# Kernel optimization log

Measured on AMD Instinct MI355X. Metric: run time of the kernel, lower is better.

## Reference

```python
import jax, jax.numpy as jnp
import numpy as np

DIM_IN, DIM_OUT, DIM_CTX = 128, 256, 259
B, N, S_CTX = 32, 2048, 1
BN_EPS = 1e-5


def setup_inputs() -> dict:
    key = jax.random.key(0)
    ks = jax.random.split(key, 12)
    s = 0.02
    return {
        "ctx": jax.random.normal(ks[0], (B, S_CTX, DIM_CTX), jnp.float32),
        "x": jax.random.normal(ks[1], (B, N, DIM_IN), jnp.float32),
        "W_layer": jax.random.normal(ks[2], (DIM_OUT, DIM_IN), jnp.float32) * s,
        "b_layer": jax.random.normal(ks[3], (DIM_OUT,), jnp.float32) * s,
        "W_hbias": jax.random.normal(ks[4], (DIM_OUT, DIM_CTX), jnp.float32) * s,
        "W_gate": jax.random.normal(ks[5], (DIM_OUT, DIM_CTX), jnp.float32) * s,
        "b_gate": jax.random.normal(ks[6], (DIM_OUT,), jnp.float32) * s,
        "W_k": jax.random.normal(ks[7], (DIM_OUT, DIM_CTX - 3), jnp.float32) * s,
        "W_v": jax.random.normal(ks[8], (DIM_OUT, DIM_CTX - 3), jnp.float32) * s,
        "W_tc": jax.random.normal(ks[9], (DIM_OUT, DIM_OUT), jnp.float32) * s,
        "b_tc": jax.random.normal(ks[10], (DIM_OUT,), jnp.float32) * s,
        "bn_gamma": jnp.ones((N,), jnp.float32),
        "bn_beta": jnp.zeros((N,), jnp.float32),
    }


def reference(ctx, x, W_layer, b_layer, W_hbias, W_gate, b_gate, W_k, W_v, W_tc, b_tc, bn_gamma, bn_beta):
    # FiLM gate / bias from context: [B, 1, dim_out]
    gate = jax.nn.sigmoid(jnp.einsum('bsc,oc->bso', ctx, W_gate) + b_gate)
    bias = jnp.einsum('bsc,oc->bso', ctx, W_hbias)

    # main linear: [B, N, dim_out]
    x1 = jnp.einsum('bni,oi->bno', x, W_layer) + b_layer

    # channel attention from shape context (drop last 3 ctx dims)
    shape = ctx[:, :, : ctx.shape[2] - 3]                      # [B, S, C-3]
    shape_k = jnp.einsum('bsc,oc->bos', shape, W_k)            # [B, dim_out, S]
    shape_v = jnp.einsum('bsc,oc->bso', shape, W_v)            # [B, S, dim_out]
    energy = jnp.einsum('bos,bse->boe', shape_k, shape_v)      # [B, dim_out, dim_out]
    attention = jax.nn.softmax(energy, axis=-1)
    attention = attention / (1e-9 + attention.sum(axis=1, keepdims=True))

    # channel mixing: [B, N, dim_out]
    x_r = jnp.einsum('bno,boe->bne', x1, attention)

    # trans_conv + BatchNorm1d(N) (train-mode batch stats over dims (0, 2)) + ReLU
    t = jnp.einsum('bno,eo->bne', x1 - x_r, W_tc) + b_tc       # [B, N, dim_out]
    mean = t.mean(axis=(0, 2), keepdims=True)                  # per point-channel
    var = t.var(axis=(0, 2), keepdims=True)                    # biased variance
    t = (t - mean) * jax.lax.rsqrt(var + BN_EPS)
    t = t * bn_gamma[None, :, None] + bn_beta[None, :, None]
    x_r = jax.nn.relu(t)

    xo = x1 + x_r
    return xo * gate + bias
```

## Files before the change

### kernel.cpp

```cpp
#include <hip/hip_runtime.h>
#include <hip/hip_bf16.h>

#define BB   32
#define NN   2048
#define DIN  128
#define DOUT 256
#define DCTX 259

#define OFF_AB   0u
#define OFF_WMB  16777216u
#define OFF_WLB  17301504u
#define OFF_WLTB 17317888u
#define OFF_WTCB 17334272u
#define OFF_G    17367040u
#define OFF_HB   17375232u
#define OFF_TB   17383424u
#define OFF_P1   17655296u
#define OFF_P2   17720832u
#define OFF_KS   17786368u
#define OFF_VS   17794560u

typedef short bf16x8 __attribute__((ext_vector_type(8)));
typedef float f32x4  __attribute__((ext_vector_type(4)));

static __device__ inline unsigned short f2bf(float f) {
    __hip_bfloat16 h = __float2bfloat16(f);
    return *(unsigned short*)&h;
}
static __device__ inline float bf2f(unsigned short u) {
    unsigned v = ((unsigned)u) << 16;
    float f;
    __builtin_memcpy(&f, &v, 4);
    return f;
}

__global__ __launch_bounds__(256) void kW(const float* __restrict__ Wl,
                                          const float* __restrict__ Wtc,
                                          const float* __restrict__ Wk,
                                          const float* __restrict__ Wv,
                                          const float* __restrict__ Wg,
                                          const float* __restrict__ Whb,
                                          const float* __restrict__ ctx,
                                          const float* __restrict__ bg,
                                          float* __restrict__ ws) {
    const unsigned bb = blockIdx.x, t = threadIdx.x;
    __shared__ float ctxs[32][260];
    __shared__ float wt[16][260];

    if (bb < 8u) {
        unsigned base = bb * 8192u;
        unsigned short* dst = (unsigned short*)(ws + OFF_WTCB);
#pragma unroll
        for (int j = 0; j < 32; j++) {
            unsigned i = base + (unsigned)j * 256u + t;
            dst[i] = f2bf(Wtc[i]);
        }
        return;
    } else if (bb == 8u) {
        unsigned short* dst = (unsigned short*)(ws + OFF_WLTB);
        for (unsigned idx = t; idx < 32768u; idx += 256u) {
            unsigned i = idx >> 8, o = idx & 255u;
            dst[idx] = f2bf(Wl[o * 128u + i]);
        }
        return;
    } else if (bb == 9u) {
        unsigned short* dst = (unsigned short*)(ws + OFF_WLB);
        for (unsigned idx = t; idx < 32768u; idx += 256u) dst[idx] = f2bf(Wl[idx]);
        return;
    }

    const int j = bb - 10;
    const int m = j >> 4;
    const int o0 = (j & 15) * 16;
    const float* Wm; int C;
    if (m == 0)      { Wm = Wk;  C = 256; }
    else if (m == 1) { Wm = Wv;  C = 256; }
    else if (m == 2) { Wm = Wg;  C = DCTX; }
    else             { Wm = Whb; C = DCTX; }

    for (int i = t; i < 32 * 260; i += 256) {
        int b2 = i / 260, c = i - b2 * 260;
        ctxs[b2][c] = (c < DCTX) ? ctx[b2 * DCTX + c] : 0.f;
    }
    for (int i = t; i < 16 * C; i += 256) {
        int r = i / C, c = i - r * C;
        wt[r][c] = Wm[(size_t)(o0 + r) * C + c];
    }
    __syncthreads();

    const int ol = t & 15, b2 = t >> 4;
    float s0 = 0.f, s1 = 0.f;
#pragma unroll 8
    for (int c = 0; c < C; c++) {
        float w = wt[ol][c];
        s0 += w * ctxs[b2][c];
        s1 += w * ctxs[b2 + 16][c];
    }
    const int o = o0 + ol;
    if (m == 0) {
        ws[OFF_KS + b2 * DOUT + o] = s0;
        ws[OFF_KS + (b2 + 16) * DOUT + o] = s1;
    } else if (m == 1) {
        ws[OFF_VS + b2 * DOUT + o] = s0;
        ws[OFF_VS + (b2 + 16) * DOUT + o] = s1;
    } else if (m == 2) {
        float bgo = bg[o];
        ws[OFF_G + b2 * DOUT + o] = 1.f / (1.f + __expf(-(s0 + bgo)));
        ws[OFF_G + (b2 + 16) * DOUT + o] = 1.f / (1.f + __expf(-(s1 + bgo)));
    } else {
        ws[OFF_HB + b2 * DOUT + o] = s0;
        ws[OFF_HB + (b2 + 16) * DOUT + o] = s1;
    }
}

__global__ __launch_bounds__(1024) void kP(float* __restrict__ ws) {
    const int b = blockIdx.x, t = threadIdx.x;
    const int o = t & 255, q = t >> 8;
    __shared__ __align__(16) float ks[256], vs[256], rms[256], ris[256];
    __shared__ float pm[1024], ps[1024];
    if (t < 256)            ks[t] = ws[OFF_KS + b * DOUT + t];
    else if (t < 512)       vs[t - 256] = ws[OFF_VS + b * DOUT + (t - 256)];
    __syncthreads();

    const float ko = ks[o];
    const float4* vs4 = (const float4*)vs;
    float pmax = -1e30f;
#pragma unroll 4
    for (int j = q * 16; j < q * 16 + 16; j++) {
        float4 v = vs4[j];
        pmax = fmaxf(pmax, fmaxf(fmaxf(ko * v.x, ko * v.y), fmaxf(ko * v.z, ko * v.w)));
    }
    pm[q * 256 + o] = pmax;
    __syncthreads();
    float m = fmaxf(fmaxf(pm[o], pm[256 + o]), fmaxf(pm[512 + o], pm[768 + o]));
    float psum = 0.f;
#pragma unroll 4
    for (int j = q * 16; j < q * 16 + 16; j++) {
        float4 v = vs4[j];
        psum += __expf(ko * v.x - m) + __expf(ko * v.y - m)
              + __expf(ko * v.z - m) + __expf(ko * v.w - m);
    }
    ps[q * 256 + o] = psum;
    __syncthreads();
    float ri = 1.f / (ps[o] + ps[256 + o] + ps[512 + o] + ps[768 + o]);
    if (q == 0) { rms[o] = m; ris[o] = ri; }
    __syncthreads();

    const float ve = vs[o];
    float cp = 0.f;
#pragma unroll 4
    for (int o2 = q * 64; o2 < q * 64 + 64; o2++)
        cp += __expf(ks[o2] * ve - rms[o2]) * ris[o2];
    pm[q * 256 + o] = cp;
    __syncthreads();
    float ci = 1.f / (1e-9f + pm[o] + pm[256 + o] + pm[512 + o] + pm[768 + o]);
    unsigned short* Ab = (unsigned short*)(ws + OFF_AB) + (size_t)b * 65536u;
#pragma unroll 4
    for (int o2 = q * 64; o2 < q * 64 + 64; o2++) {
        float a = __expf(ks[o2] * ve - rms[o2]) * ris[o2] * ci;
        Ab[o2 * 256 + o] = f2bf(a);
    }
}

__global__ __launch_bounds__(512) void k45(const float* __restrict__ bl,
                                           const float* __restrict__ btc,
                                           float* __restrict__ ws) {
    const int t = threadIdx.x, wid = t >> 6, l = t & 63;
    const int b = blockIdx.y, et = blockIdx.x;
    const int lrow = l & 15, lk = l >> 4;
    __shared__ unsigned short Mt[64 * 256];
    const unsigned short* Wtcb = (const unsigned short*)(ws + OFF_WTCB);

    {
        const unsigned short* Ab = (const unsigned short*)(ws + OFF_AB) + (size_t)b * 65536u;
        const int w_r = wid >> 2, w_c = wid & 3;
        const int rbase = et * 64 + w_r * 32;
        const int colbase = w_c * 64;
        f32x4 acc[2][4];
#pragma unroll
        for (int i = 0; i < 2; i++)
#pragma unroll
            for (int c = 0; c < 4; c++) acc[i][c] = (f32x4){0.f, 0.f, 0.f, 0.f};
        const unsigned short* ar0 = Wtcb + (rbase + lrow) * 256;
#pragma unroll
        for (int kk = 0; kk < 8; kk++) {
            int ko = kk * 32 + lk * 8;
            bf16x8 a0 = *(const bf16x8*)(ar0 + ko);
            bf16x8 a1 = *(const bf16x8*)(ar0 + 16 * 256 + ko);
            bf16x8 bfr[4];
#pragma unroll
            for (int c = 0; c < 4; c++)
                bfr[c] = *(const bf16x8*)(Ab + (colbase + c * 16 + lrow) * 256 + ko);
#pragma unroll
            for (int c = 0; c < 4; c++) {
                acc[0][c] = __builtin_amdgcn_mfma_f32_16x16x32_bf16(a0, bfr[c], acc[0][c], 0, 0, 0);
                acc[1][c] = __builtin_amdgcn_mfma_f32_16x16x32_bf16(a1, bfr[c], acc[1][c], 0, 0, 0);
            }
        }
#pragma unroll
        for (int t2 = 0; t2 < 2; t2++)
#pragma unroll
            for (int c = 0; c < 4; c++)
#pragma unroll
                for (int r = 0; r < 4; r++) {
                    int grow = rbase + t2 * 16 + lk * 4 + r;
                    int col = colbase + c * 16 + lrow;
                    float idv = bf2f(Wtcb[grow * 256 + col]);
                    int rl = grow - et * 64;
                    Mt[rl * 256 + (col ^ ((rl & 7) << 3))] = f2bf(idv - acc[t2][c][r]);
                }
    }
    __syncthreads();
    {
        const unsigned short* Wltb = (const unsigned short*)(ws + OFF_WLTB);
        const int w_r = wid >> 2, w_c = wid & 3;
        const int rl0 = w_r * 32;
        const int colb = w_c * 32;
        f32x4 acc[2][2];
#pragma unroll
        for (int i = 0; i < 2; i++)
#pragma unroll
            for (int c = 0; c < 2; c++) acc[i][c] = (f32x4){0.f, 0.f, 0.f, 0.f};
        const int arow0 = rl0 + lrow, arow1 = rl0 + 16 + lrow;
        const int asw0 = (arow0 & 7) << 3, asw1 = (arow1 & 7) << 3;
#pragma unroll
        for (int kk = 0; kk < 8; kk++) {
            int ko = kk * 32 + lk * 8;
            bf16x8 a0 = *(const bf16x8*)(Mt + arow0 * 256 + (ko ^ asw0));
            bf16x8 a1 = *(const bf16x8*)(Mt + arow1 * 256 + (ko ^ asw1));
            bf16x8 bfr[2];
#pragma unroll
            for (int c = 0; c < 2; c++)
                bfr[c] = *(const bf16x8*)(Wltb + (colb + c * 16 + lrow) * 256 + ko);
#pragma unroll
            for (int c = 0; c < 2; c++) {
                acc[0][c] = __builtin_amdgcn_mfma_f32_16x16x32_bf16(a0, bfr[c], acc[0][c], 0, 0, 0);
                acc[1][c] = __builtin_amdgcn_mfma_f32_16x16x32_bf16(a1, bfr[c], acc[1][c], 0, 0, 0);
            }
        }
        unsigned short* WMBp = (unsigned short*)(ws + OFF_WMB) + (size_t)b * 32768u;
#pragma unroll
        for (int t2 = 0; t2 < 2; t2++)
#pragma unroll
            for (int c = 0; c < 2; c++)
#pragma unroll
                for (int r = 0; r < 4; r++) {
                    int row = et * 64 + rl0 + t2 * 16 + lk * 4 + r;
                    int col = colb + c * 16 + lrow;
                    WMBp[row * 128 + col] = f2bf(acc[t2][c][r]);
                }
    }
    if (t < 64) {
        const int rl = t;
        const int sw = (rl & 7) << 3;
        float s = 0.f;
#pragma unroll 4
        for (int j = 0; j < 32; j++) {
            bf16x8 ch = *(const bf16x8*)(Mt + rl * 256 + ((j * 8) ^ sw));
#pragma unroll
            for (int u = 0; u < 8; u++) s += bl[j * 8 + u] * bf2f((unsigned short)ch[u]);
        }
        ws[OFF_TB + b * DOUT + et * 64 + rl] = s + btc[et * 64 + rl];
    }
}

#define LDP 136

__global__ __launch_bounds__(256) void kS(const float* __restrict__ x,
                                          float* __restrict__ ws) {
    const int t = threadIdx.x;
    const int wid = t >> 6, l = t & 63;
    const int b = blockIdx.x, nt = blockIdx.y;
    const int n0 = nt * 64;
    const int lrow = l & 15, lk = l >> 4;
    __shared__ unsigned short xs[64 * LDP];
    __shared__ float sp1[4][64], sp2[4][64];

    const float4* xg = (const float4*)(x + (size_t)(b * NN + n0) * DIN);
#pragma unroll
    for (int it = 0; it < 8; it++) {
        int idx = it * 256 + t;
        int row = idx >> 5, kq = idx & 31;
        float4 v = xg[idx];
        ushort4 u;
        u.x = f2bf(v.x); u.y = f2bf(v.y); u.z = f2bf(v.z); u.w = f2bf(v.w);
        *(ushort4*)(xs + row * LDP + kq * 4) = u;
    }
    __syncthreads();

    const int colbase = wid * 64;
    f32x4 acc[4][4];
#pragma unroll
    for (int rt = 0; rt < 4; rt++)
#pragma unroll
        for (int ct = 0; ct < 4; ct++) acc[rt][ct] = (f32x4){0.f, 0.f, 0.f, 0.f};
    {
        const unsigned short* wb = (const unsigned short*)(ws + OFF_WMB) + (size_t)b * 32768u;
#pragma unroll
        for (int kk = 0; kk < 4; kk++) {
            int ko = kk * 32 + lk * 8;
            bf16x8 a[4];
#pragma unroll
            for (int rt = 0; rt < 4; rt++)
                a[rt] = *(const bf16x8*)(xs + (rt * 16 + lrow) * LDP + ko);
            bf16x8 bf[4];
#pragma unroll
            for (int ct = 0; ct < 4; ct++)
                bf[ct] = *(const bf16x8*)(wb + (size_t)(colbase + ct * 16 + lrow) * DIN + ko);
#pragma unroll
            for (int rt = 0; rt < 4; rt++)
#pragma unroll
                for (int ct = 0; ct < 4; ct++)
                    acc[rt][ct] = __builtin_amdgcn_mfma_f32_16x16x32_bf16(a[rt], bf[ct], acc[rt][ct], 0, 0, 0);
        }
#pragma unroll
        for (int ct = 0; ct < 4; ct++) {
            float bv = ws[OFF_TB + b * DOUT + colbase + ct * 16 + lrow];
#pragma unroll
            for (int rt = 0; rt < 4; rt++)
#pragma unroll
                for (int r = 0; r < 4; r++) acc[rt][ct][r] += bv;
        }
    }

    float s1[4][4], s2[4][4];
#pragma unroll
    for (int rt = 0; rt < 4; rt++)
#pragma unroll
        for (int r = 0; r < 4; r++) { s1[rt][r] = 0.f; s2[rt][r] = 0.f; }
#pragma unroll
    for (int rt = 0; rt < 4; rt++)
#pragma unroll
        for (int ct = 0; ct < 4; ct++)
#pragma unroll
            for (int r = 0; r < 4; r++) {
                float v = acc[rt][ct][r];
                s1[rt][r] += v; s2[rt][r] += v * v;
            }
#pragma unroll
    for (int off = 1; off < 16; off <<= 1) {
#pragma unroll
        for (int rt = 0; rt < 4; rt++)
#pragma unroll
            for (int r = 0; r < 4; r++) {
                s1[rt][r] += __shfl_xor(s1[rt][r], off, 64);
                s2[rt][r] += __shfl_xor(s2[rt][r], off, 64);
            }
    }
    if (lrow == 0) {
#pragma unroll
        for (int rt = 0; rt < 4; rt++)
#pragma unroll
            for (int r = 0; r < 4; r++) {
                int nidx = rt * 16 + lk * 4 + r;
                sp1[wid][nidx] = s1[rt][r];
                sp2[wid][nidx] = s2[rt][r];
            }
    }
    __syncthreads();
    if (t < 64) {
        float S1 = sp1[0][t] + sp1[1][t] + sp1[2][t] + sp1[3][t];
        float S2 = sp2[0][t] + sp2[1][t] + sp2[2][t] + sp2[3][t];
        ws[OFF_P1 + (size_t)b * NN + n0 + t] = S1;
        ws[OFF_P2 + (size_t)b * NN + n0 + t] = S2;
    }
}

__global__ __launch_bounds__(256) void kF(const float* __restrict__ x,
                                          const float* __restrict__ bl,
                                          const float* __restrict__ gamma,
                                          const float* __restrict__ beta,
                                          float* __restrict__ out,
                                          float* __restrict__ ws) {
    const int t = threadIdx.x;
    const int wid = t >> 6, l = t & 63;
    const int b = blockIdx.x;
    const int nt = blockIdx.y;
    const int n0 = nt * 64;
    const int lrow = l & 15, lk = l >> 4;
    __shared__ unsigned short xs[64 * LDP];
    __shared__ float sq1[4][64], sq2[4][64];
    __shared__ float scs[64], shs[64];

    const float4* xg = (const float4*)(x + (size_t)(b * NN + n0) * DIN);
    float4 xv[8];
#pragma unroll
    for (int it = 0; it < 8; it++) xv[it] = xg[it * 256 + t];

    {
        int n = t & 63, g = t >> 6;
        float S1 = 0.f, S2 = 0.f;
#pragma unroll
        for (int b2 = g * 8; b2 < g * 8 + 8; b2++) {
            S1 += ws[OFF_P1 + (size_t)b2 * NN + n0 + n];
            S2 += ws[OFF_P2 + (size_t)b2 * NN + n0 + n];
        }
        sq1[g][n] = S1; sq2[g][n] = S2;
    }
    __syncthreads();
    if (t < 64) {
        float S1 = sq1[0][t] + sq1[1][t] + sq1[2][t] + sq1[3][t];
        float S2 = sq2[0][t] + sq2[1][t] + sq2[2][t] + sq2[3][t];
        float mean = S1 * (1.f / 8192.f);
        float var  = S2 * (1.f / 8192.f) - mean * mean;
        float sc = gamma[n0 + t] * rsqrtf(fmaxf(var, 0.f) + 1e-5f);
        scs[t] = sc;
        shs[t] = beta[n0 + t] - mean * sc;
    }
#pragma unroll
    for (int it = 0; it < 8; it++) {
        int idx = it * 256 + t;
        int row = idx >> 5, kq = idx & 31;
        ushort4 u;
        u.x = f2bf(xv[it].x); u.y = f2bf(xv[it].y); u.z = f2bf(xv[it].z); u.w = f2bf(xv[it].w);
        *(ushort4*)(xs + row * LDP + kq * 4) = u;
    }
    __syncthreads();

    const int colbase = wid * 64;

    f32x4 acc[4][4], acc0[4][4];
#pragma unroll
    for (int rt = 0; rt < 4; rt++)
#pragma unroll
        for (int ct = 0; ct < 4; ct++) {
            acc[rt][ct]  = (f32x4){0.f, 0.f, 0.f, 0.f};
            acc0[rt][ct] = (f32x4){0.f, 0.f, 0.f, 0.f};
        }
    {
        const unsigned short* wbM = (const unsigned short*)(ws + OFF_WMB) + (size_t)b * 32768u;
        const unsigned short* wbL = (const unsigned short*)(ws + OFF_WLB);
#pragma unroll
        for (int kk = 0; kk < 4; kk++) {
            int ko = kk * 32 + lk * 8;
            bf16x8 a[4];
#pragma unroll
            for (int rt = 0; rt < 4; rt++)
                a[rt] = *(const bf16x8*)(xs + (rt * 16 + lrow) * LDP + ko);
            bf16x8 bf[4];
#pragma unroll
            for (int ct = 0; ct < 4; ct++)
                bf[ct] = *(const bf16x8*)(wbM + (size_t)(colbase + ct * 16 + lrow) * DIN + ko);
#pragma unroll
            for (int rt = 0; rt < 4; rt++)
#pragma unroll
                for (int ct = 0; ct < 4; ct++)
                    acc[rt][ct] = __builtin_amdgcn_mfma_f32_16x16x32_bf16(a[rt], bf[ct], acc[rt][ct], 0, 0, 0);
#pragma unroll
            for (int ct = 0; ct < 4; ct++)
                bf[ct] = *(const bf16x8*)(wbL + (size_t)(colbase + ct * 16 + lrow) * DIN + ko);
#pragma unroll
            for (int rt = 0; rt < 4; rt++)
#pragma unroll
                for (int ct = 0; ct < 4; ct++)
                    acc0[rt][ct] = __builtin_amdgcn_mfma_f32_16x16x32_bf16(a[rt], bf[ct], acc0[rt][ct], 0, 0, 0);
        }
#pragma unroll
        for (int ct = 0; ct < 4; ct++) {
            float bvM = ws[OFF_TB + b * DOUT + colbase + ct * 16 + lrow];
            float bvL = bl[colbase + ct * 16 + lrow];
#pragma unroll
            for (int rt = 0; rt < 4; rt++)
#pragma unroll
                for (int r = 0; r < 4; r++) {
                    acc[rt][ct][r]  += bvM;
                    acc0[rt][ct][r] += bvL;
                }
        }
    }

    float gv[4], hbv[4];
#pragma unroll
    for (int ct = 0; ct < 4; ct++) {
        int o = colbase + ct * 16 + lrow;
        gv[ct]  = ws[OFF_G  + b * DOUT + o];
        hbv[ct] = ws[OFF_HB + b * DOUT + o];
    }
#pragma unroll
    for (int rt = 0; rt < 4; rt++)
#pragma unroll
        for (int r = 0; r < 4; r++) {
            int nidx = rt * 16 + lk * 4 + r;
            float sc = scs[nidx], sh = shs[nidx];
            int n = n0 + nidx;
#pragma unroll
            for (int ct = 0; ct < 4; ct++) {
                int o = colbase + ct * 16 + lrow;
                float rv = fmaxf(acc[rt][ct][r] * sc + sh, 0.f);
                out[(size_t)((b * NN + n) * DOUT) + o] = (acc0[rt][ct][r] + rv) * gv[ct] + hbv[ct];
            }
        }
}

extern "C" void kernel_launch(void* const* d_in, const int* in_sizes, int n_in,
                              void* d_out, int out_size, void* d_ws, size_t ws_size,
                              hipStream_t stream) {
    const float* ctx   = (const float*)d_in[0];
    const float* x     = (const float*)d_in[1];
    const float* Wl    = (const float*)d_in[2];
    const float* bl    = (const float*)d_in[3];
    const float* Whb   = (const float*)d_in[4];
    const float* Wg    = (const float*)d_in[5];
    const float* bg    = (const float*)d_in[6];
    const float* Wk    = (const float*)d_in[7];
    const float* Wv    = (const float*)d_in[8];
    const float* Wtc   = (const float*)d_in[9];
    const float* btc   = (const float*)d_in[10];
    const float* gamma = (const float*)d_in[11];
    const float* beta  = (const float*)d_in[12];
    float* out = (float*)d_out;
    float* ws  = (float*)d_ws;

    kW  <<<74, 256, 0, stream>>>(Wl, Wtc, Wk, Wv, Wg, Whb, ctx, bg, ws);
    kP  <<<BB, 1024, 0, stream>>>(ws);
    k45 <<<dim3(4, BB), 512, 0, stream>>>(bl, btc, ws);
    kS  <<<dim3(BB, 32), 256, 0, stream>>>(x, ws);
    kF  <<<dim3(BB, 32), 256, 0, stream>>>(x, bl, gamma, beta, out, ws);
}
```

Before: 208.7 us.

## Fuse stats and final kernels via per-tile atomic counter grid barrier

Merges the statistics pass and the final output pass into one kernel. Each block loads and converts x once, computes the trans_conv GEMM to get per-point partial sums, publishes them, and increments a per-n-tile atomic counter. It then computes the x1 GEMM while waiting for all 32 batch blocks of the same n-tile to arrive. This removes a second read of x, a repeated GEMM and one kernel launch. The cost is a spin-wait that relies on all 1024 blocks being co-resident or on the scheduler's dispatch order, with some deadlock risk if they are not.

New measurement: 208.0 us. About the same (-0.4%).

```diff
diff --git a/kernel.cpp b/kernel.cpp
--- a/kernel.cpp
+++ b/kernel.cpp
@@ -19,6 +19,7 @@
 #define OFF_P2   17720832u
 #define OFF_KS   17786368u
 #define OFF_VS   17794560u
+#define OFF_CNT  17802752u
 
 typedef short bf16x8 __attribute__((ext_vector_type(8)));
 typedef float f32x4  __attribute__((ext_vector_type(4)));
@@ -66,6 +67,10 @@
     } else if (bb == 9u) {
         unsigned short* dst = (unsigned short*)(ws + OFF_WLB);
         for (unsigned idx = t; idx < 32768u; idx += 256u) dst[idx] = f2bf(Wl[idx]);
+        return;
+    } else if (bb == 74u) {
+        unsigned* c = (unsigned*)(ws + OFF_CNT);
+        for (unsigned i = t; i < 1024u; i += 256u) c[i] = 0u;
         return;
     }
 
@@ -266,15 +271,21 @@
 
 #define LDP 136
 
-__global__ __launch_bounds__(256) void kS(const float* __restrict__ x,
-                                          float* __restrict__ ws) {
+__global__ __launch_bounds__(256) void kFS(const float* __restrict__ x,
+                                           const float* __restrict__ bl,
+                                           const float* __restrict__ gamma,
+                                           const float* __restrict__ beta,
+                                           float* __restrict__ out,
+                                           float* __restrict__ ws) {
     const int t = threadIdx.x;
     const int wid = t >> 6, l = t & 63;
-    const int b = blockIdx.x, nt = blockIdx.y;
+    const int b = blockIdx.x;
+    const int nt = blockIdx.y;
     const int n0 = nt * 64;
     const int lrow = l & 15, lk = l >> 4;
     __shared__ unsigned short xs[64 * LDP];
     __shared__ float sp1[4][64], sp2[4][64];
+    __shared__ float scs[64], shs[64];
 
     const float4* xg = (const float4*)(x + (size_t)(b * NN + n0) * DIN);
 #pragma unroll
@@ -289,13 +300,14 @@
     __syncthreads();
 
     const int colbase = wid * 64;
+
     f32x4 acc[4][4];
 #pragma unroll
     for (int rt = 0; rt < 4; rt++)
 #pragma unroll
         for (int ct = 0; ct < 4; ct++) acc[rt][ct] = (f32x4){0.f, 0.f, 0.f, 0.f};
     {
-        const unsigned short* wb = (const unsigned short*)(ws + OFF_WMB) + (size_t)b * 32768u;
+        const unsigned short* wbM = (const unsigned short*)(ws + OFF_WMB) + (size_t)b * 32768u;
 #pragma unroll
         for (int kk = 0; kk < 4; kk++) {
             int ko = kk * 32 + lk * 8;
@@ -306,7 +318,7 @@
             bf16x8 bf[4];
 #pragma unroll
             for (int ct = 0; ct < 4; ct++)
-                bf[ct] = *(const bf16x8*)(wb + (size_t)(colbase + ct * 16 + lrow) * DIN + ko);
+                bf[ct] = *(const bf16x8*)(wbM + (size_t)(colbase + ct * 16 + lrow) * DIN + ko);
 #pragma unroll
             for (int rt = 0; rt < 4; rt++)
 #pragma unroll
@@ -323,39 +335,41 @@
         }
     }
 
-    float s1[4][4], s2[4][4];
-#pragma unroll
-    for (int rt = 0; rt < 4; rt++)
-#pragma unroll
-        for (int r = 0; r < 4; r++) { s1[rt][r] = 0.f; s2[rt][r] = 0.f; }
-#pragma unroll
-    for (int rt = 0; rt < 4; rt++)
-#pragma unroll
-        for (int ct = 0; ct < 4; ct++)
-#pragma unroll
-            for (int r = 0; r < 4; r++) {
-                float v = acc[rt][ct][r];
-                s1[rt][r] += v; s2[rt][r] += v * v;
-            }
-#pragma unroll
-    for (int off = 1; off < 16; off <<= 1) {
+    {
+        float s1[4][4], s2[4][4];
 #pragma unroll
         for (int rt = 0; rt < 4; rt++)
 #pragma unroll
-            for (int r = 0; r < 4; r++) {
-                s1[rt][r] += __shfl_xor(s1[rt][r], off, 64);
-                s2[rt][r] += __shfl_xor(s2[rt][r], off, 64);
-            }
-    }
-    if (lrow == 0) {
+            for (int r = 0; r < 4; r++) { s1[rt][r] = 0.f; s2[rt][r] = 0.f; }
 #pragma unroll
         for (int rt = 0; rt < 4; rt++)
 #pragma unroll
-            for (int r = 0; r < 4; r++) {
-                int nidx = rt * 16 + lk * 4 + r;
-                sp1[wid][nidx] = s1[rt][r];
-                sp2[wid][nidx] = s2[rt][r];
-            }
+            for (int ct = 0; ct < 4; ct++)
+#pragma unroll
+                for (int r = 0; r < 4; r++) {
+                    float v = acc[rt][ct][r];
+                    s1[rt][r] += v; s2[rt][r] += v * v;
+                }
+#pragma unroll
+        for (int off = 1; off < 16; off <<= 1) {
+#pragma unroll
+            for (int rt = 0; rt < 4; rt++)
+#pragma unroll
+                for (int r = 0; r < 4; r++) {
+                    s1[rt][r] += __shfl_xor(s1[rt][r], off, 64);
+                    s2[rt][r] += __shfl_xor(s2[rt][r], off, 64);
+                }
+        }
+        if (lrow == 0) {
+#pragma unroll
+            for (int rt = 0; rt < 4; rt++)
+#pragma unroll
+                for (int r = 0; r < 4; r++) {
+                    int nidx = rt * 16 + lk * 4 + r;
+                    sp1[wid][nidx] = s1[rt][r];
+                    sp2[wid][nidx] = s2[rt][r];
+                }
+        }
     }
     __syncthreads();
     if (t < 64) {
@@ -364,28 +378,51 @@
         ws[OFF_P1 + (size_t)b * NN + n0 + t] = S1;
         ws[OFF_P2 + (size_t)b * NN + n0 + t] = S2;
     }
-}
-
-__global__ __launch_bounds__(256) void kF(const float* __restrict__ x,
-                                          const float* __restrict__ bl,
-                                          const float* __restrict__ gamma,
-                                          const float* __restrict__ beta,
-                                          float* __restrict__ out,
-                                          float* __restrict__ ws) {
-    const int t = threadIdx.x;
-    const int wid = t >> 6, l = t & 63;
-    const int b = blockIdx.x;
-    const int nt = blockIdx.y;
-    const int n0 = nt * 64;
-    const int lrow = l & 15, lk = l >> 4;
-    __shared__ unsigned short xs[64 * LDP];
-    __shared__ float sq1[4][64], sq2[4][64];
-    __shared__ float scs[64], shs[64];
-
-    const float4* xg = (const float4*)(x + (size_t)(b * NN + n0) * DIN);
-    float4 xv[8];
-#pragma unroll
-    for (int it = 0; it < 8; it++) xv[it] = xg[it * 256 + t];
+    __syncthreads();
+
+    unsigned* cnt = (unsigned*)(ws + OFF_CNT) + (size_t)nt * 32;
+    if (t == 0)
+        __hip_atomic_fetch_add(cnt, 1u, __ATOMIC_RELEASE, __HIP_MEMORY_SCOPE_AGENT);
+
+    f32x4 acc0[4][4];
+#pragma unroll
+    for (int rt = 0; rt < 4; rt++)
+#pragma unroll
+        for (int ct = 0; ct < 4; ct++) acc0[rt][ct] = (f32x4){0.f, 0.f, 0.f, 0.f};
+    {
+        const unsigned short* wbL = (const unsigned short*)(ws + OFF_WLB);
+#pragma unroll
+        for (int kk = 0; kk < 4; kk++) {
+            int ko = kk * 32 + lk * 8;
+            bf16x8 a[4];
+#pragma unroll
+            for (int rt = 0; rt < 4; rt++)
+                a[rt] = *(const bf16x8*)(xs + (rt * 16 + lrow) * LDP + ko);
+            bf16x8 bf[4];
+#pragma unroll
+            for (int ct = 0; ct < 4; ct++)
+                bf[ct] = *(const bf16x8*)(wbL + (size_t)(colbase + ct * 16 + lrow) * DIN + ko);
+#pragma unroll
+            for (int rt = 0; rt < 4; rt++)
+#pragma unroll
+                for (int ct = 0; ct < 4; ct++)
+                    acc0[rt][ct] = __builtin_amdgcn_mfma_f32_16x16x32_bf16(a[rt], bf[ct], acc0[rt][ct], 0, 0, 0);
+        }
+#pragma unroll
+        for (int ct = 0; ct < 4; ct++) {
+            float bv = bl[colbase + ct * 16 + lrow];
+#pragma unroll
+            for (int rt = 0; rt < 4; rt++)
+#pragma unroll
+                for (int r = 0; r < 4; r++) acc0[rt][ct][r] += bv;
+        }
+    }
+
+    if (t == 0) {
+        while (__hip_atomic_load(cnt, __ATOMIC_ACQUIRE, __HIP_MEMORY_SCOPE_AGENT) < (unsigned)BB)
+            __builtin_amdgcn_s_sleep(32);
+    }
+    __syncthreads();
 
     {
         int n = t & 63, g = t >> 6;
@@ -395,79 +432,19 @@
             S1 += ws[OFF_P1 + (size_t)b2 * NN + n0 + n];
             S2 += ws[OFF_P2 + (size_t)b2 * NN + n0 + n];
         }
-        sq1[g][n] = S1; sq2[g][n] = S2;
+        sp1[g][n] = S1; sp2[g][n] = S2;
     }
     __syncthreads();
     if (t < 64) {
-        float S1 = sq1[0][t] + sq1[1][t] + sq1[2][t] + sq1[3][t];
-        float S2 = sq2[0][t] + sq2[1][t] + sq2[2][t] + sq2[3][t];
+        float S1 = sp1[0][t] + sp1[1][t] + sp1[2][t] + sp1[3][t];
+        float S2 = sp2[0][t] + sp2[1][t] + sp2[2][t] + sp2[3][t];
         float mean = S1 * (1.f / 8192.f);
         float var  = S2 * (1.f / 8192.f) - mean * mean;
         float sc = gamma[n0 + t] * rsqrtf(fmaxf(var, 0.f) + 1e-5f);
         scs[t] = sc;
         shs[t] = beta[n0 + t] - mean * sc;
     }
-#pragma unroll
-    for (int it = 0; it < 8; it++) {
-        int idx = it * 256 + t;
-        int row = idx >> 5, kq = idx & 31;
-        ushort4 u;
-        u.x = f2bf(xv[it].x); u.y = f2bf(xv[it].y); u.z = f2bf(xv[it].z); u.w = f2bf(xv[it].w);
-        *(ushort4*)(xs + row * LDP + kq * 4) = u;
-    }
-    __syncthreads();
-
-    const int colbase = wid * 64;
-
-    f32x4 acc[4][4], acc0[4][4];
-#pragma unroll
-    for (int rt = 0; rt < 4; rt++)
-#pragma unroll
-        for (int ct = 0; ct < 4; ct++) {
-            acc[rt][ct]  = (f32x4){0.f, 0.f, 0.f, 0.f};
-            acc0[rt][ct] = (f32x4){0.f, 0.f, 0.f, 0.f};
-        }
-    {
-        const unsigned short* wbM = (const unsigned short*)(ws + OFF_WMB) + (size_t)b * 32768u;
-        const unsigned short* wbL = (const unsigned short*)(ws + OFF_WLB);
-#pragma unroll
-        for (int kk = 0; kk < 4; kk++) {
-            int ko = kk * 32 + lk * 8;
-            bf16x8 a[4];
-#pragma unroll
-            for (int rt = 0; rt < 4; rt++)
-                a[rt] = *(const bf16x8*)(xs + (rt * 16 + lrow) * LDP + ko);
-            bf16x8 bf[4];
-#pragma unroll
-            for (int ct = 0; ct < 4; ct++)
-                bf[ct] = *(const bf16x8*)(wbM + (size_t)(colbase + ct * 16 + lrow) * DIN + ko);
-#pragma unroll
-            for (int rt = 0; rt < 4; rt++)
-#pragma unroll
-                for (int ct = 0; ct < 4; ct++)
-                    acc[rt][ct] = __builtin_amdgcn_mfma_f32_16x16x32_bf16(a[rt], bf[ct], acc[rt][ct], 0, 0, 0);
-#pragma unroll
-            for (int ct = 0; ct < 4; ct++)
-                bf[ct] = *(const bf16x8*)(wbL + (size_t)(colbase + ct * 16 + lrow) * DIN + ko);
-#pragma unroll
-            for (int rt = 0; rt < 4; rt++)
-#pragma unroll
-                for (int ct = 0; ct < 4; ct++)
-                    acc0[rt][ct] = __builtin_amdgcn_mfma_f32_16x16x32_bf16(a[rt], bf[ct], acc0[rt][ct], 0, 0, 0);
-        }
-#pragma unroll
-        for (int ct = 0; ct < 4; ct++) {
-            float bvM = ws[OFF_TB + b * DOUT + colbase + ct * 16 + lrow];
-            float bvL = bl[colbase + ct * 16 + lrow];
-#pragma unroll
-            for (int rt = 0; rt < 4; rt++)
-#pragma unroll
-                for (int r = 0; r < 4; r++) {
-                    acc[rt][ct][r]  += bvM;
-                    acc0[rt][ct][r] += bvL;
-                }
-        }
-    }
+    __syncthreads();
 
     float gv[4], hbv[4];
 #pragma unroll
@@ -511,9 +488,8 @@
     float* out = (float*)d_out;
     float* ws  = (float*)d_ws;
 
-    kW  <<<74, 256, 0, stream>>>(Wl, Wtc, Wk, Wv, Wg, Whb, ctx, bg, ws);
+    kW  <<<75, 256, 0, stream>>>(Wl, Wtc, Wk, Wv, Wg, Whb, ctx, bg, ws);
     kP  <<<BB, 1024, 0, stream>>>(ws);
     k45 <<<dim3(4, BB), 512, 0, stream>>>(bl, btc, ws);
-    kS  <<<dim3(BB, 32), 256, 0, stream>>>(x, ws);
-    kF  <<<dim3(BB, 32), 256, 0, stream>>>(x, bl, gamma, beta, out, ws);
-}
+    kFS <<<dim3(BB, 32), 256, 0, stream>>>(x, bl, gamma, beta, out, ws);
+}
```

## Fuse attention softmax into Wtc-attention GEMM, compute attention tiles on the fly

Applied to the files above, without the earlier changes.

Removes the separate kP kernel that built and wrote the full 32x256x256 bf16 attention matrix to global memory. Each kQ block now recomputes the softmax row statistics and column normalisers in shared memory and generates attention tiles per k-step into an LDS buffer feeding the MFMA. This drops a 4 MB global write/read round trip and one launch. In exchange the statistics are computed redundantly by the 4 blocks per batch, there are extra syncs per k-step, and exp work moves inside the GEMM loop.

Result: faster. 200.7 us (-3.8%).

```diff
diff --git a/kernel.cpp b/kernel.cpp
--- a/kernel.cpp
+++ b/kernel.cpp
@@ -7,18 +7,17 @@
 #define DOUT 256
 #define DCTX 259
 
-#define OFF_AB   0u
-#define OFF_WMB  16777216u
-#define OFF_WLB  17301504u
-#define OFF_WLTB 17317888u
-#define OFF_WTCB 17334272u
-#define OFF_G    17367040u
-#define OFF_HB   17375232u
-#define OFF_TB   17383424u
-#define OFF_P1   17655296u
-#define OFF_P2   17720832u
-#define OFF_KS   17786368u
-#define OFF_VS   17794560u
+#define OFF_WMB  0u
+#define OFF_WLB  524288u
+#define OFF_WLTB 540672u
+#define OFF_WTCB 557056u
+#define OFF_G    589824u
+#define OFF_HB   598016u
+#define OFF_TB   606208u
+#define OFF_P1   614400u
+#define OFF_P2   679936u
+#define OFF_KS   745472u
+#define OFF_VS   753664u
 
 typedef short bf16x8 __attribute__((ext_vector_type(8)));
 typedef float f32x4  __attribute__((ext_vector_type(4)));
@@ -113,67 +112,58 @@
     }
 }
 
-__global__ __launch_bounds__(1024) void kP(float* __restrict__ ws) {
-    const int b = blockIdx.x, t = threadIdx.x;
-    const int o = t & 255, q = t >> 8;
-    __shared__ __align__(16) float ks[256], vs[256], rms[256], ris[256];
-    __shared__ float pm[1024], ps[1024];
-    if (t < 256)            ks[t] = ws[OFF_KS + b * DOUT + t];
-    else if (t < 512)       vs[t - 256] = ws[OFF_VS + b * DOUT + (t - 256)];
-    __syncthreads();
-
-    const float ko = ks[o];
-    const float4* vs4 = (const float4*)vs;
-    float pmax = -1e30f;
-#pragma unroll 4
-    for (int j = q * 16; j < q * 16 + 16; j++) {
-        float4 v = vs4[j];
-        pmax = fmaxf(pmax, fmaxf(fmaxf(ko * v.x, ko * v.y), fmaxf(ko * v.z, ko * v.w)));
-    }
-    pm[q * 256 + o] = pmax;
-    __syncthreads();
-    float m = fmaxf(fmaxf(pm[o], pm[256 + o]), fmaxf(pm[512 + o], pm[768 + o]));
-    float psum = 0.f;
-#pragma unroll 4
-    for (int j = q * 16; j < q * 16 + 16; j++) {
-        float4 v = vs4[j];
-        psum += __expf(ko * v.x - m) + __expf(ko * v.y - m)
-              + __expf(ko * v.z - m) + __expf(ko * v.w - m);
-    }
-    ps[q * 256 + o] = psum;
-    __syncthreads();
-    float ri = 1.f / (ps[o] + ps[256 + o] + ps[512 + o] + ps[768 + o]);
-    if (q == 0) { rms[o] = m; ris[o] = ri; }
-    __syncthreads();
-
-    const float ve = vs[o];
-    float cp = 0.f;
-#pragma unroll 4
-    for (int o2 = q * 64; o2 < q * 64 + 64; o2++)
-        cp += __expf(ks[o2] * ve - rms[o2]) * ris[o2];
-    pm[q * 256 + o] = cp;
-    __syncthreads();
-    float ci = 1.f / (1e-9f + pm[o] + pm[256 + o] + pm[512 + o] + pm[768 + o]);
-    unsigned short* Ab = (unsigned short*)(ws + OFF_AB) + (size_t)b * 65536u;
-#pragma unroll 4
-    for (int o2 = q * 64; o2 < q * 64 + 64; o2++) {
-        float a = __expf(ks[o2] * ve - rms[o2]) * ris[o2] * ci;
-        Ab[o2 * 256 + o] = f2bf(a);
-    }
-}
-
-__global__ __launch_bounds__(512) void k45(const float* __restrict__ bl,
-                                           const float* __restrict__ btc,
-                                           float* __restrict__ ws) {
+__global__ __launch_bounds__(512) void kQ(const float* __restrict__ bl,
+                                          const float* __restrict__ btc,
+                                          float* __restrict__ ws) {
     const int t = threadIdx.x, wid = t >> 6, l = t & 63;
     const int b = blockIdx.y, et = blockIdx.x;
     const int lrow = l & 15, lk = l >> 4;
     __shared__ unsigned short Mt[64 * 256];
+    __shared__ unsigned short Abc[256 * 40];
+    __shared__ __align__(16) float ks[256], vs[256], rms[256], ris[256], ci[256];
+    __shared__ float pm[512], ps[512];
     const unsigned short* Wtcb = (const unsigned short*)(ws + OFF_WTCB);
 
+    if (t < 256)      ks[t] = ws[OFF_KS + b * DOUT + t];
+    else              vs[t - 256] = ws[OFF_VS + b * DOUT + (t - 256)];
+    __syncthreads();
+    const int o = t & 255, q = t >> 8;
     {
-        const unsigned short* Ab = (const unsigned short*)(ws + OFF_AB) + (size_t)b * 65536u;
-        const int w_r = wid >> 2, w_c = wid & 3;
+        const float ko_ = ks[o];
+        const float4* vs4 = (const float4*)vs;
+        float pmax = -1e30f;
+#pragma unroll 4
+        for (int j = q * 32; j < q * 32 + 32; j++) {
+            float4 v = vs4[j];
+            pmax = fmaxf(pmax, fmaxf(fmaxf(ko_ * v.x, ko_ * v.y), fmaxf(ko_ * v.z, ko_ * v.w)));
+        }
+        pm[t] = pmax;
+        __syncthreads();
+        float m = fmaxf(pm[o], pm[256 + o]);
+        float psum = 0.f;
+#pragma unroll 4
+        for (int j = q * 32; j < q * 32 + 32; j++) {
+            float4 v = vs4[j];
+            psum += __expf(ko_ * v.x - m) + __expf(ko_ * v.y - m)
+                  + __expf(ko_ * v.z - m) + __expf(ko_ * v.w - m);
+        }
+        ps[t] = psum;
+        __syncthreads();
+        if (q == 0) { rms[o] = m; ris[o] = 1.f / (ps[o] + ps[256 + o]); }
+        __syncthreads();
+        const float ve = vs[o];
+        float cp = 0.f;
+#pragma unroll 4
+        for (int o2 = q * 128; o2 < q * 128 + 128; o2++)
+            cp += __expf(ks[o2] * ve - rms[o2]) * ris[o2];
+        pm[t] = cp;
+        __syncthreads();
+        if (q == 0) ci[o] = 1.f / (1e-9f + pm[o] + pm[256 + o]);
+        __syncthreads();
+    }
+
+    const int w_r = wid >> 2, w_c = wid & 3;
+    {
         const int rbase = et * 64 + w_r * 32;
         const int colbase = w_c * 64;
         f32x4 acc[2][4];
@@ -182,20 +172,28 @@
 #pragma unroll
             for (int c = 0; c < 4; c++) acc[i][c] = (f32x4){0.f, 0.f, 0.f, 0.f};
         const unsigned short* ar0 = Wtcb + (rbase + lrow) * 256;
-#pragma unroll
+        const int o2 = t & 255, h = t >> 8;
+        const float k2 = ks[o2], rm = rms[o2], ri = ris[o2];
         for (int kk = 0; kk < 8; kk++) {
+#pragma unroll 8
+            for (int j = 0; j < 16; j++) {
+                int e = kk * 32 + h * 16 + j;
+                Abc[o2 * 40 + h * 16 + j] = f2bf(__expf(k2 * vs[e] - rm) * ri * ci[e]);
+            }
+            __syncthreads();
             int ko = kk * 32 + lk * 8;
             bf16x8 a0 = *(const bf16x8*)(ar0 + ko);
             bf16x8 a1 = *(const bf16x8*)(ar0 + 16 * 256 + ko);
             bf16x8 bfr[4];
 #pragma unroll
             for (int c = 0; c < 4; c++)
-                bfr[c] = *(const bf16x8*)(Ab + (colbase + c * 16 + lrow) * 256 + ko);
+                bfr[c] = *(const bf16x8*)(Abc + (colbase + c * 16 + lrow) * 40 + lk * 8);
 #pragma unroll
             for (int c = 0; c < 4; c++) {
                 acc[0][c] = __builtin_amdgcn_mfma_f32_16x16x32_bf16(a0, bfr[c], acc[0][c], 0, 0, 0);
                 acc[1][c] = __builtin_amdgcn_mfma_f32_16x16x32_bf16(a1, bfr[c], acc[1][c], 0, 0, 0);
             }
+            __syncthreads();
         }
 #pragma unroll
         for (int t2 = 0; t2 < 2; t2++)
@@ -213,7 +211,6 @@
     __syncthreads();
     {
         const unsigned short* Wltb = (const unsigned short*)(ws + OFF_WLTB);
-        const int w_r = wid >> 2, w_c = wid & 3;
         const int rl0 = w_r * 32;
         const int colb = w_c * 32;
         f32x4 acc[2][2];
@@ -511,9 +508,8 @@
     float* out = (float*)d_out;
     float* ws  = (float*)d_ws;
 
-    kW  <<<74, 256, 0, stream>>>(Wl, Wtc, Wk, Wv, Wg, Whb, ctx, bg, ws);
-    kP  <<<BB, 1024, 0, stream>>>(ws);
-    k45 <<<dim3(4, BB), 512, 0, stream>>>(bl, btc, ws);
-    kS  <<<dim3(BB, 32), 256, 0, stream>>>(x, ws);
-    kF  <<<dim3(BB, 32), 256, 0, stream>>>(x, bl, gamma, beta, out, ws);
-}
+    kW <<<74, 256, 0, stream>>>(Wl, Wtc, Wk, Wv, Wg, Whb, ctx, bg, ws);
+    kQ <<<dim3(4, BB), 512, 0, stream>>>(bl, btc, ws);
+    kS <<<dim3(BB, 32), 256, 0, stream>>>(x, ws);
+    kF <<<dim3(BB, 32), 256, 0, stream>>>(x, bl, gamma, beta, out, ws);
+}
```
